# Performance work log

Measured on AMD Instinct MI355X. Metric: run time of the kernel, lower is better.

## Reference

```python
import jax, jax.numpy as jnp
import numpy as np

IFZ = 256      # in_features
SFZ = 1280     # sequence_features
AHZ = 8        # attention heads
AFZ = 64       # attention feature dim per head
NRES = 20      # canonical_num_residues
SCALE = float(np.sqrt(AFZ))
RESID = float(np.sqrt(2.0))
EPS = 1e-6


def _ln(x, s, b, eps=1e-5):
    m = jnp.mean(x, axis=-1, keepdims=True)
    v = jnp.var(x, axis=-1, keepdims=True)
    return (x - m) / jnp.sqrt(v + eps) * s + b


def setup_inputs() -> dict:
    key = jax.random.key(0)
    ks = jax.random.split(key, 20)
    N, B, S = 4096, 4, 512
    HD = AHZ * AFZ
    w = lambda k, shp: (jax.random.normal(k, shp, jnp.float32) * 0.02)
    d = {}
    d["x"] = jax.random.normal(ks[0], (N, IFZ), jnp.float32)
    d["packed_sequence_emb"] = jax.random.normal(ks[1], (B, S, SFZ), jnp.float32)
    d["packed_sequence_mask"] = jnp.ones((B, S), jnp.float32)
    d["prot_mask"] = jnp.arange(N, dtype=jnp.int32)
    d["batch"] = jax.random.randint(ks[2], (N,), 0, B, jnp.int32)
    # projections (bias=False)
    d["Wq"] = w(ks[3], (HD, IFZ))
    d["Wk"] = w(ks[4], (HD, SFZ))
    d["Wv"] = w(ks[5], (HD, SFZ))
    # ag: LayerNorm(HD) -> Linear(HD, IFZ, bias=False) (dropout = identity at eval)
    d["ag_ln_s"] = jnp.ones((HD,), jnp.float32)
    d["ag_ln_b"] = jnp.zeros((HD,), jnp.float32)
    d["Wag"] = w(ks[6], (IFZ, HD))
    d["res_ln_s"] = jnp.ones((3, IFZ), jnp.float32)
    d["res_ln_b"] = jnp.zeros((3, IFZ), jnp.float32)
    d["res_w1"] = w(ks[7], (3, IFZ, IFZ))
    d["res_b1"] = jnp.zeros((3, IFZ), jnp.float32)
    d["res_w2"] = w(ks[8], (3, IFZ, IFZ))
    d["res_b2"] = jnp.zeros((3, IFZ), jnp.float32)
    d["head_w"] = w(ks[9], (NRES, IFZ))
    d["head_b"] = jnp.zeros((NRES,), jnp.float32)
    # output LayerNorm en
    d["en_s"] = jnp.ones((IFZ,), jnp.float32)
    d["en_b"] = jnp.zeros((IFZ,), jnp.float32)
    return d


def _forward(x, emb, mask, prot_mask, batch, Wq, Wk, Wv, ag_ln_s, ag_ln_b, Wag,
             res_ln_s, res_ln_b, res_w1, res_b1, res_w2, res_b2,
             head_w, head_b, en_s, en_b):
    N = x.shape[0]
    B, S = emb.shape[:2]
    b_idx = batch[prot_mask]                      # [M]
    xp = x[prot_mask]                             # [M, IFZ]
    M = xp.shape[0]
    q = (xp @ Wq.T).reshape(M, AHZ, AFZ)          # [M,H,D]
    k = (emb @ Wk.T).reshape(B, S, AHZ, AFZ)      # [B,S,H,D]
    v = (emb @ Wv.T).reshape(B, S, AHZ, AFZ)
    # score vs every protein, then pick own protein (avoids materializing [M,S,H,D] gather)
    scores_all = jnp.einsum('mhd,bshd->mbsh', q, k) / SCALE          # [M,B,S,H]
    sel = b_idx[:, None, None, None]
    scores = jnp.take_along_axis(scores_all, sel, axis=1)[:, 0]       # [M,S,H]
    mb = mask[b_idx][:, :, None]                                      # [M,S,1]
    # padded_sequence_softmax: softmax over S, zero pads, renormalize
    sm = jax.nn.softmax(scores, axis=1) * mb
    w = sm / (jnp.sum(sm, axis=1, keepdims=True) + EPS)               # [M,S,H]
    feat_all = jnp.einsum('msh,bshd->mbhd', w, v)                     # [M,B,H,D]
    feat = jnp.take_along_axis(feat_all, sel, axis=1)[:, 0]
    feat = feat.reshape(M, AHZ * AFZ)
    ag = _ln(feat, ag_ln_s, ag_ln_b) @ Wag.T                          # [M, IFZ]
    # seq_aa_head on the scattered new features (identical to ag for unique prot_mask)
    h = ag
    for i in range(3):
        y = _ln(h, res_ln_s[i], res_ln_b[i])
        y = jax.nn.relu(y @ res_w1[i].T + res_b1[i])
        y = y @ res_w2[i].T + res_b2[i]
        h = (h + y) / RESID
    logits = h @ head_w.T + head_b                                     # [M, NRES]
    new_features = jnp.zeros_like(x).at[prot_mask].set(ag)
    seq_aa_logits = jnp.zeros((N, NRES), x.dtype).at[prot_mask].set(logits)
    unpacked_scores = jnp.zeros((N, S, AHZ), x.dtype).at[prot_mask].set(scores)
    out_x = _ln(x + new_features / RESID, en_s, en_b)
    return out_x, seq_aa_logits, unpacked_scores


def reference(x, packed_sequence_emb, packed_sequence_mask, prot_mask, batch,
              Wq, Wk, Wv, ag_ln_s, ag_ln_b, Wag,
              res_ln_s, res_ln_b, res_w1, res_b1, res_w2, res_b2,
              head_w, head_b, en_s, en_b):
    return _forward(x, packed_sequence_emb, packed_sequence_mask, prot_mask, batch,
                    Wq, Wk, Wv, ag_ln_s, ag_ln_b, Wag,
                    res_ln_s, res_ln_b, res_w1, res_b1, res_w2, res_b2,
                    head_w, head_b, en_s, en_b)
```

## Files before the change

kernel.cpp:

```cpp
#include <hip/hip_runtime.h>
#include <math.h>


typedef short bf8 __attribute__((ext_vector_type(8)));
typedef short bf4 __attribute__((ext_vector_type(4)));
typedef float f32x4 __attribute__((ext_vector_type(4)));
typedef unsigned short u16;

constexpr int LDT = 40;
enum { EPI_NONE = 0, EPI_BIAS_RELU = 1, EPI_BIAS = 2, EPI_RESID = 3 };
#define RSQRT2 0.70710678118654752f

__device__ __forceinline__ u16 f2bf(float f) {
  unsigned int u = __builtin_bit_cast(unsigned int, f);
  unsigned int r = u + 0x7fffu + ((u >> 16) & 1u);
  return (u16)(r >> 16);
}
__device__ __forceinline__ float bf2f(u16 v) {
  return __builtin_bit_cast(float, (unsigned int)v << 16);
}
__device__ __forceinline__ f32x4 mfma16(bf8 a, bf8 b, f32x4 c) {
  return __builtin_amdgcn_mfma_f32_16x16x32_bf16(a, b, c, 0, 0, 0);
}

struct CvtDesc { const float* src; u16* dst; int n; };
struct CvtArgs { CvtDesc d[8]; };

__global__ __launch_bounds__(256) void cvt_k(CvtArgs a) {
  CvtDesc d = a.d[blockIdx.z];
  int i = (blockIdx.x * 256 + threadIdx.x) * 8;
  if (i >= d.n) return;
  f32x4 v0 = *(const f32x4*)(d.src + i);
  f32x4 v1 = *(const f32x4*)(d.src + i + 4);
  bf8 o;
  o[0] = (short)f2bf(v0[0]); o[1] = (short)f2bf(v0[1]);
  o[2] = (short)f2bf(v0[2]); o[3] = (short)f2bf(v0[3]);
  o[4] = (short)f2bf(v1[0]); o[5] = (short)f2bf(v1[1]);
  o[6] = (short)f2bf(v1[2]); o[7] = (short)f2bf(v1[3]);
  *(bf8*)(d.dst + i) = o;
}

template <int EPI, bool BFOUT>
__global__ __launch_bounds__(256) void mgemm2(
    const u16* __restrict__ A, const u16* __restrict__ B,
    void* __restrict__ Cv, int M, int N, int K, int lda, int ldb, int ldc,
    const float* __restrict__ bias, const float* __restrict__ Hin,
    const int* __restrict__ gatherA, const int* __restrict__ scatterC) {
  __shared__ __align__(16) u16 As[128 * LDT];
  __shared__ __align__(16) u16 Bs[64 * LDT];
  const int tid = threadIdx.x;
  const int m0 = blockIdx.y * 128, n0 = blockIdx.x * 64;
  const int wave = tid >> 6, lane = tid & 63;
  const int wm = (wave & 1) * 64, wn = (wave >> 1) * 32;
  const int lrow = lane & 15, quad = lane >> 4;
  const int srow = tid >> 2, skq = tid & 3;

  int gr0 = m0 + srow, gr1 = m0 + srow + 64;
  int ar0 = (gr0 < M) ? (gatherA ? gatherA[gr0] : gr0) : -1;
  int ar1 = (gr1 < M) ? (gatherA ? gatherA[gr1] : gr1) : -1;
  const u16* Ap0 = (ar0 >= 0) ? A + (size_t)ar0 * lda + skq * 8 : nullptr;
  const u16* Ap1 = (ar1 >= 0) ? A + (size_t)ar1 * lda + skq * 8 : nullptr;
  const u16* Bp = (n0 + srow < N) ? B + (size_t)(n0 + srow) * ldb + skq * 8 : nullptr;
  u16* AsW0 = &As[srow * LDT + skq * 8];
  u16* AsW1 = &As[(srow + 64) * LDT + skq * 8];
  u16* BsW = &Bs[srow * LDT + skq * 8];

  f32x4 acc[4][2];
#pragma unroll
  for (int i = 0; i < 4; ++i)
#pragma unroll
    for (int j = 0; j < 2; ++j) acc[i][j] = (f32x4){0.f, 0.f, 0.f, 0.f};
  const bf8 z8 = {0, 0, 0, 0, 0, 0, 0, 0};

  for (int k0 = 0; k0 < K; k0 += 32) {
    bf8 a0 = Ap0 ? *(const bf8*)(Ap0 + k0) : z8;
    bf8 a1 = Ap1 ? *(const bf8*)(Ap1 + k0) : z8;
    bf8 bv = Bp ? *(const bf8*)(Bp + k0) : z8;
    *(bf8*)AsW0 = a0;
    *(bf8*)AsW1 = a1;
    *(bf8*)BsW = bv;
    __syncthreads();
    bf8 af[4], bfr[2];
#pragma unroll
    for (int i = 0; i < 4; ++i)
      af[i] = *(const bf8*)&As[(wm + i * 16 + lrow) * LDT + quad * 8];
#pragma unroll
    for (int j = 0; j < 2; ++j)
      bfr[j] = *(const bf8*)&Bs[(wn + j * 16 + lrow) * LDT + quad * 8];
#pragma unroll
    for (int i = 0; i < 4; ++i)
#pragma unroll
      for (int j = 0; j < 2; ++j) acc[i][j] = mfma16(af[i], bfr[j], acc[i][j]);
    __syncthreads();
  }

  float* Cf = (float*)Cv;
  u16* Cb = (u16*)Cv;
#pragma unroll
  for (int i = 0; i < 4; ++i) {
#pragma unroll
    for (int r = 0; r < 4; ++r) {
      int row = m0 + wm + i * 16 + quad * 4 + r;
      if (row >= M) continue;
      if (gatherA && gatherA[row] < 0) continue;
      int orow = scatterC ? scatterC[row] : row;
#pragma unroll
      for (int j = 0; j < 2; ++j) {
        int col = n0 + wn + j * 16 + lrow;
        if (col >= N) continue;
        float v = acc[i][j][r];
        if (EPI == EPI_BIAS_RELU) v = fmaxf(v + bias[col], 0.f);
        else if (EPI == EPI_BIAS) v += bias[col];
        else if (EPI == EPI_RESID) v = (Hin[(size_t)row * ldc + col] + v + bias[col]) * RSQRT2;
        if (BFOUT) Cb[(size_t)orow * ldc + col] = f2bf(v);
        else Cf[(size_t)orow * ldc + col] = v;
      }
    }
  }
}

__global__ __launch_bounds__(256) void vtrans(const u16* __restrict__ KV,
                                              u16* __restrict__ VT) {
  __shared__ u16 t[32][33];
  int b = blockIdx.z;
  int s0 = blockIdx.x * 32, d0 = blockIdx.y * 32;
  int tx = threadIdx.x & 31, ty = threadIdx.x >> 5;
#pragma unroll
  for (int i = 0; i < 32; i += 8)
    t[ty + i][tx] = KV[(size_t)(b * 512 + s0 + ty + i) * 1024 + 512 + d0 + tx];
  __syncthreads();
#pragma unroll
  for (int i = 0; i < 32; i += 8)
    VT[(size_t)(b * 512 + d0 + ty + i) * 512 + s0 + tx] = t[tx][ty + i];
}

constexpr int WST = 520;
constexpr int QST = 72;

__global__ __launch_bounds__(256) void attn_fused(
    const u16* __restrict__ Q, const u16* __restrict__ KV,
    const u16* __restrict__ VT, const int* __restrict__ list,
    const float* __restrict__ mask, u16* __restrict__ packed,
    u16* __restrict__ feat, int N) {
  const int b = blockIdx.y >> 3, h = blockIdx.y & 7;
  const int mt = blockIdx.x;
  const int* lst = list + (size_t)b * N + mt * 32;
  if (lst[0] < 0) return;

  __shared__ __align__(16) u16 Ws[32 * WST];
  __shared__ __align__(16) u16 Qs[32 * QST];
  __shared__ __align__(16) u16 KVs[64 * QST];
  __shared__ __align__(16) float mk[8][68];
  __shared__ int mS[32];

  const int tid = threadIdx.x;
  const int wave = tid >> 6, lane = tid & 63;
  const int wm = (wave & 1) * 16, wns = (wave >> 1) * 32;
  const int lrow = lane & 15, quad = lane >> 4;
  const bf8 z8 = {0, 0, 0, 0, 0, 0, 0, 0};

  if (tid < 32) mS[tid] = lst[tid];
  {
    int p = tid >> 5, j = (tid & 31) * 2;
    *(float2*)&mk[p][j] = *(const float2*)&mask[(size_t)b * 512 + p * 64 + j];
  }
  {
    int qr = tid >> 3, kq = tid & 7;
    int m = lst[qr];
    *(bf8*)&Qs[qr * QST + kq * 8] =
        (m >= 0) ? *(const bf8*)(Q + (size_t)m * 512 + h * 64 + kq * 8) : z8;
  }
  __syncthreads();

  const bf8 qa0 = *(const bf8*)&Qs[(wm + lrow) * QST + 0 + quad * 8];
  const bf8 qa1 = *(const bf8*)&Qs[(wm + lrow) * QST + 32 + quad * 8];

  const u16* KVb = KV + (size_t)(b * 512) * 1024 + h * 64;
  for (int st = 0; st < 8; ++st) {
#pragma unroll
    for (int i = 0; i < 2; ++i) {
      int c = tid * 2 + i;
      int sr = c >> 3, kq = c & 7;
      *(bf8*)&KVs[sr * QST + kq * 8] =
          *(const bf8*)(KVb + (size_t)(st * 64 + sr) * 1024 + kq * 8);
    }
    __syncthreads();
    f32x4 acc0 = {0.f, 0.f, 0.f, 0.f}, acc1 = acc0;
    {
      bf8 b00 = *(const bf8*)&KVs[(wns + lrow) * QST + quad * 8];
      bf8 b10 = *(const bf8*)&KVs[(wns + 16 + lrow) * QST + quad * 8];
      bf8 b01 = *(const bf8*)&KVs[(wns + lrow) * QST + 32 + quad * 8];
      bf8 b11 = *(const bf8*)&KVs[(wns + 16 + lrow) * QST + 32 + quad * 8];
      acc0 = mfma16(qa0, b00, acc0);
      acc1 = mfma16(qa0, b10, acc1);
      acc0 = mfma16(qa1, b01, acc0);
      acc1 = mfma16(qa1, b11, acc1);
    }
#pragma unroll
    for (int r = 0; r < 4; ++r) {
      int lr = wm + quad * 4 + r;
      Ws[lr * WST + st * 64 + wns + lrow] = f2bf(acc0[r] * 0.125f);
      Ws[lr * WST + st * 64 + wns + 16 + lrow] = f2bf(acc1[r] * 0.125f);
    }
    __syncthreads();
  }

  {
    const int row = tid >> 3, part = tid & 7;
    u16* wrow = &Ws[row * WST + part * 64];
    const int mm = mS[row];
    bf8 w[8];
    float mx = -1e30f;
#pragma unroll
    for (int v = 0; v < 8; ++v) {
      w[v] = *(const bf8*)(wrow + v * 8);
#pragma unroll
      for (int j = 0; j < 8; ++j) mx = fmaxf(mx, bf2f((u16)w[v][j]));
    }
    if (mm >= 0) {
      u16* prow = packed + ((size_t)h * N + mm) * 512 + part * 64;
#pragma unroll
      for (int v = 0; v < 8; ++v) *(bf8*)(prow + v * 8) = w[v];
    }
#pragma unroll
    for (int d = 1; d < 8; d <<= 1) mx = fmaxf(mx, __shfl_xor(mx, d));
    float se = 0.f, ms = 0.f;
#pragma unroll
    for (int v = 0; v < 8; ++v) {
      f32x4 m0 = *(const f32x4*)&mk[part][v * 8];
      f32x4 m1 = *(const f32x4*)&mk[part][v * 8 + 4];
#pragma unroll
      for (int j = 0; j < 8; ++j) {
        float e = __expf(bf2f((u16)w[v][j]) - mx);
        se += e;
        ms += e * (j < 4 ? m0[j] : m1[j - 4]);
      }
    }
#pragma unroll
    for (int d = 1; d < 8; d <<= 1) {
      se += __shfl_xor(se, d);
      ms += __shfl_xor(ms, d);
    }
    float iv = 1.0f / (ms + 1e-6f * se);
#pragma unroll
    for (int v = 0; v < 8; ++v) {
      f32x4 m0 = *(const f32x4*)&mk[part][v * 8];
      f32x4 m1 = *(const f32x4*)&mk[part][v * 8 + 4];
      bf8 o;
#pragma unroll
      for (int j = 0; j < 8; ++j) {
        float e = __expf(bf2f((u16)w[v][j]) - mx);
        o[j] = (short)f2bf(e * (j < 4 ? m0[j] : m1[j - 4]) * iv);
      }
      *(bf8*)(wrow + v * 8) = o;
    }
  }
  __syncthreads();

  f32x4 acc0 = {0.f, 0.f, 0.f, 0.f}, acc1 = acc0;
  const u16* VTb = VT + (size_t)(b * 512 + h * 64) * 512;
  for (int s0 = 0; s0 < 512; s0 += 64) {
#pragma unroll
    for (int i = 0; i < 2; ++i) {
      int c = tid * 2 + i;
      int sr = c >> 3, kq = c & 7;
      *(bf8*)&KVs[sr * QST + kq * 8] =
          *(const bf8*)(VTb + (size_t)sr * 512 + s0 + kq * 8);
    }
    __syncthreads();
#pragma unroll
    for (int k0 = 0; k0 < 64; k0 += 32) {
      bf8 a = *(const bf8*)&Ws[(wm + lrow) * WST + s0 + k0 + quad * 8];
      bf8 b0 = *(const bf8*)&KVs[(wns + lrow) * QST + k0 + quad * 8];
      bf8 b1 = *(const bf8*)&KVs[(wns + 16 + lrow) * QST + k0 + quad * 8];
      acc0 = mfma16(a, b0, acc0);
      acc1 = mfma16(a, b1, acc1);
    }
    __syncthreads();
  }
#pragma unroll
  for (int r = 0; r < 4; ++r) {
    int lr = wm + quad * 4 + r;
    int mm = mS[lr];
    if (mm < 0) continue;
    u16* frow = feat + (size_t)mm * 512 + h * 64;
    frow[wns + lrow] = f2bf(acc0[r]);
    frow[wns + 16 + lrow] = f2bf(acc1[r]);
  }
}

__global__ __launch_bounds__(256) void unpack_k(const u16* __restrict__ packed,
                                                const int* __restrict__ pm,
                                                float* __restrict__ out_sc,
                                                int N) {
  __shared__ u16 Ls[8 * 520];
  int m = blockIdx.x, tid = threadIdx.x;
  int h = tid >> 5, c = (tid & 31) * 16;
  const u16* row = packed + ((size_t)h * N + m) * 512 + c;
  *(bf8*)&Ls[h * 520 + c] = *(const bf8*)row;
  *(bf8*)&Ls[h * 520 + c + 8] = *(const bf8*)(row + 8);
  __syncthreads();
  float* orow = out_sc + (size_t)pm[m] * 4096;
#pragma unroll
  for (int i = 0; i < 16; ++i) {
    int e = tid + i * 256;
    orow[e] = bf2f(Ls[(e & 7) * 520 + (e >> 3)]);
  }
}

template <int W, bool BFIN, bool BFOUT>
__global__ __launch_bounds__(256) void ln_k(const void* __restrict__ in,
                                            void* __restrict__ out,
                                            const float* __restrict__ g,
                                            const float* __restrict__ bb) {
  constexpr int PT = W / 256;
  __shared__ float red[256];
  int row = blockIdx.x, tid = threadIdx.x;
  float v[PT];
  float s = 0.f, sq = 0.f;
#pragma unroll
  for (int p = 0; p < PT; ++p) {
    int c = tid + p * 256;
    v[p] = BFIN ? bf2f(((const u16*)in)[(size_t)row * W + c])
                : ((const float*)in)[(size_t)row * W + c];
    s += v[p];
    sq += v[p] * v[p];
  }
  red[tid] = s;
  __syncthreads();
  for (int off = 128; off; off >>= 1) {
    if (tid < off) red[tid] += red[tid + off];
    __syncthreads();
  }
  float mean = red[0] * (1.0f / W);
  __syncthreads();
  red[tid] = sq;
  __syncthreads();
  for (int off = 128; off; off >>= 1) {
    if (tid < off) red[tid] += red[tid + off];
    __syncthreads();
  }
  float var = red[0] * (1.0f / W) - mean * mean;
  float is = 1.0f / sqrtf(var + 1e-5f);
#pragma unroll
  for (int p = 0; p < PT; ++p) {
    int c = tid + p * 256;
    float o = (v[p] - mean) * is * g[c] + bb[c];
    if (BFOUT) ((u16*)out)[(size_t)row * W + c] = f2bf(o);
    else ((float*)out)[(size_t)row * W + c] = o;
  }
}

constexpr int HST = 268;
constexpr int AST = 280;

__global__ __launch_bounds__(256) void mlp_fused(
    const float* __restrict__ AG, const float* __restrict__ rls,
    const float* __restrict__ rlb, const u16* __restrict__ rw1,
    const float* __restrict__ rb1, const u16* __restrict__ rw2,
    const float* __restrict__ rb2, const float* __restrict__ hw,
    const float* __restrict__ hb, const int* __restrict__ pm,
    float* __restrict__ out_lg) {
  __shared__ __align__(16) float Hs[32 * HST];
  __shared__ __align__(16) u16 As[32 * AST];
  const int tid = threadIdx.x;
  const int m0 = blockIdx.x * 32;
  const int wave = tid >> 6, lane = tid & 63;
  const int lrow = lane & 15, quad = lane >> 4;
  const int wn = wave * 64;
  const int row = tid >> 3, part = tid & 7;

#pragma unroll
  for (int v = 0; v < 8; ++v) {
    int c = v * 32 + part * 4;
    *(f32x4*)&Hs[row * HST + c] = *(const f32x4*)&AG[(size_t)(m0 + row) * 256 + c];
  }

  for (int layer = 0; layer < 3; ++layer) {
    __syncthreads();
    {
      float s = 0.f, sq = 0.f;
      f32x4 hv[8];
#pragma unroll
      for (int v = 0; v < 8; ++v) {
        hv[v] = *(const f32x4*)&Hs[row * HST + v * 32 + part * 4];
#pragma unroll
        for (int e = 0; e < 4; ++e) { s += hv[v][e]; sq += hv[v][e] * hv[v][e]; }
      }
#pragma unroll
      for (int d = 1; d < 8; d <<= 1) { s += __shfl_xor(s, d); sq += __shfl_xor(sq, d); }
      float mean = s * (1.0f / 256.0f);
      float var = sq * (1.0f / 256.0f) - mean * mean;
      float is = 1.0f / sqrtf(var + 1e-5f);
      const float* g = rls + layer * 256;
      const float* bb = rlb + layer * 256;
#pragma unroll
      for (int v = 0; v < 8; ++v) {
        int c = v * 32 + part * 4;
        f32x4 gv = *(const f32x4*)&g[c];
        f32x4 bv = *(const f32x4*)&bb[c];
        bf4 o;
#pragma unroll
        for (int e = 0; e < 4; ++e)
          o[e] = (short)f2bf((hv[v][e] - mean) * is * gv[e] + bv[e]);
        *(bf4*)&As[row * AST + c] = o;
      }
    }
    __syncthreads();

    {
      const u16* W = rw1 + (size_t)layer * 65536;
      f32x4 acc[2][4];
#pragma unroll
      for (int i = 0; i < 2; ++i)
#pragma unroll
        for (int j = 0; j < 4; ++j) acc[i][j] = (f32x4){0.f, 0.f, 0.f, 0.f};
#pragma unroll 4
      for (int k0 = 0; k0 < 256; k0 += 32) {
        bf8 a0 = *(const bf8*)&As[lrow * AST + k0 + quad * 8];
        bf8 a1 = *(const bf8*)&As[(16 + lrow) * AST + k0 + quad * 8];
#pragma unroll
        for (int nt = 0; nt < 4; ++nt) {
          bf8 bfr = *(const bf8*)&W[(size_t)(wn + nt * 16 + lrow) * 256 + k0 + quad * 8];
          acc[0][nt] = mfma16(a0, bfr, acc[0][nt]);
          acc[1][nt] = mfma16(a1, bfr, acc[1][nt]);
        }
      }
      __syncthreads();
      const float* b1 = rb1 + layer * 256;
#pragma unroll
      for (int mt = 0; mt < 2; ++mt)
#pragma unroll
        for (int nt = 0; nt < 4; ++nt) {
          int col = wn + nt * 16 + lrow;
          float bias = b1[col];
#pragma unroll
          for (int r = 0; r < 4; ++r) {
            int rr = mt * 16 + quad * 4 + r;
            As[rr * AST + col] = f2bf(fmaxf(acc[mt][nt][r] + bias, 0.f));
          }
        }
    }
    __syncthreads();

    {
      const u16* W = rw2 + (size_t)layer * 65536;
      f32x4 acc[2][4];
#pragma unroll
      for (int i = 0; i < 2; ++i)
#pragma unroll
        for (int j = 0; j < 4; ++j) acc[i][j] = (f32x4){0.f, 0.f, 0.f, 0.f};
#pragma unroll 4
      for (int k0 = 0; k0 < 256; k0 += 32) {
        bf8 a0 = *(const bf8*)&As[lrow * AST + k0 + quad * 8];
        bf8 a1 = *(const bf8*)&As[(16 + lrow) * AST + k0 + quad * 8];
#pragma unroll
        for (int nt = 0; nt < 4; ++nt) {
          bf8 bfr = *(const bf8*)&W[(size_t)(wn + nt * 16 + lrow) * 256 + k0 + quad * 8];
          acc[0][nt] = mfma16(a0, bfr, acc[0][nt]);
          acc[1][nt] = mfma16(a1, bfr, acc[1][nt]);
        }
      }
      const float* b2 = rb2 + layer * 256;
#pragma unroll
      for (int mt = 0; mt < 2; ++mt)
#pragma unroll
        for (int nt = 0; nt < 4; ++nt) {
          int col = wn + nt * 16 + lrow;
          float bias = b2[col];
#pragma unroll
          for (int r = 0; r < 4; ++r) {
            int rr = mt * 16 + quad * 4 + r;
            Hs[rr * HST + col] = (Hs[rr * HST + col] + acc[mt][nt][r] + bias) * RSQRT2;
          }
        }
    }
  }
  __syncthreads();

  {
    int orow = pm[m0 + row];
    const float* hrow = &Hs[row * HST];
    int c2 = part + 16;
    const float* w0 = hw + (size_t)part * 256;
    const float* w1 = hw + (size_t)(part + 8) * 256;
    const float* w2 = hw + (size_t)(part < 4 ? c2 : 0) * 256;
    float l0 = 0.f, l1 = 0.f, l2 = 0.f;
    for (int k = 0; k < 256; k += 4) {
      f32x4 h4 = *(const f32x4*)&hrow[k];
      f32x4 a4 = *(const f32x4*)&w0[k];
      f32x4 b4 = *(const f32x4*)&w1[k];
      f32x4 c4 = *(const f32x4*)&w2[k];
#pragma unroll
      for (int e = 0; e < 4; ++e) {
        l0 += h4[e] * a4[e];
        l1 += h4[e] * b4[e];
        l2 += h4[e] * c4[e];
      }
    }
    out_lg[(size_t)orow * 20 + part] = l0 + hb[part];
    out_lg[(size_t)orow * 20 + part + 8] = l1 + hb[part + 8];
    if (part < 4) out_lg[(size_t)orow * 20 + c2] = l2 + hb[c2];
  }
}

__global__ __launch_bounds__(256) void outx_k(
    const float* __restrict__ x, const float* __restrict__ ag,
    const int* __restrict__ inv, const float* __restrict__ g,
    const float* __restrict__ bb, float* __restrict__ out) {
  __shared__ float red[256];
  int n = blockIdx.x, tid = threadIdx.x;
  int mi = inv[n];
  float v = x[(size_t)n * 256 + tid];
  if (mi >= 0) v += ag[(size_t)mi * 256 + tid] * RSQRT2;
  red[tid] = v;
  __syncthreads();
  for (int off = 128; off; off >>= 1) {
    if (tid < off) red[tid] += red[tid + off];
    __syncthreads();
  }
  float mean = red[0] * (1.0f / 256.0f);
  __syncthreads();
  red[tid] = v * v;
  __syncthreads();
  for (int off = 128; off; off >>= 1) {
    if (tid < off) red[tid] += red[tid + off];
    __syncthreads();
  }
  float var = red[0] * (1.0f / 256.0f) - mean * mean;
  float is = 1.0f / sqrtf(var + 1e-5f);
  out[(size_t)n * 256 + tid] = (v - mean) * is * g[tid] + bb[tid];
}

__global__ void init_idx_k(int* __restrict__ list, int* __restrict__ inv,
                           int* __restrict__ cnt, int N, int B) {
  int i = blockIdx.x * 256 + threadIdx.x;
  if (i < B * N) list[i] = -1;
  if (i < N) inv[i] = -1;
  if (i < B) cnt[i] = 0;
}

__global__ void compact_k(const int* __restrict__ pm,
                          const int* __restrict__ batch, int* __restrict__ list,
                          int* __restrict__ inv, int* __restrict__ cnt, int N) {
  int m = blockIdx.x * 256 + threadIdx.x;
  if (m >= N) return;
  int p = pm[m];
  int b = batch[p];
  int slot = atomicAdd(&cnt[b], 1);
  list[(size_t)b * N + slot] = m;
  inv[p] = m;
}

extern "C" void kernel_launch(void* const* d_in, const int* in_sizes, int n_in,
                              void* d_out, int out_size, void* d_ws,
                              size_t ws_size, hipStream_t stream) {
  const float* x = (const float*)d_in[0];
  const float* emb = (const float*)d_in[1];
  const float* mask = (const float*)d_in[2];
  const int* pm = (const int*)d_in[3];
  const int* batch = (const int*)d_in[4];
  const float* Wq = (const float*)d_in[5];
  const float* Wk = (const float*)d_in[6];
  const float* Wv = (const float*)d_in[7];
  const float* ag_s = (const float*)d_in[8];
  const float* ag_b = (const float*)d_in[9];
  const float* Wag = (const float*)d_in[10];
  const float* rls = (const float*)d_in[11];
  const float* rlb = (const float*)d_in[12];
  const float* rw1 = (const float*)d_in[13];
  const float* rb1 = (const float*)d_in[14];
  const float* rw2 = (const float*)d_in[15];
  const float* rb2 = (const float*)d_in[16];
  const float* hw = (const float*)d_in[17];
  const float* hb = (const float*)d_in[18];
  const float* ens = (const float*)d_in[19];
  const float* enb = (const float*)d_in[20];

  const int N = in_sizes[0] / 256;
  const int B = in_sizes[2] / 512;

  char* wsb = (char*)d_ws;
  u16* embbf = (u16*)(wsb + 0);
  u16* xbf   = (u16*)(wsb + 5242880);
  u16* Wkvbf = (u16*)(wsb + 7340032);
  u16* Wqbf  = (u16*)(wsb + 9961472);
  u16* packed = (u16*)(wsb + 0);
  u16* KVbf   = (u16*)(wsb + 33554432);
  u16* Qbf    = (u16*)(wsb + 37748736);
  u16* VT     = (u16*)(wsb + 41943040);
  u16* featE  = (u16*)(wsb + 44040192);
  u16* LNF = (u16*)(wsb + 33554432);
  float* AG = (float*)(wsb + 37748736);
  u16* Wagbf = (u16*)(wsb + 48234496);
  u16* rw1bf = (u16*)(wsb + 48496640);
  u16* rw2bf = (u16*)(wsb + 48889856);
  int* list  = (int*)(wsb + 49545216);
  int* inv   = (int*)(wsb + 49610752);
  int* cnt   = (int*)(wsb + 49627136);

  float* out_x = (float*)d_out;
  float* out_lg = out_x + (size_t)N * 256;
  float* out_sc = out_lg + (size_t)N * 20;

  CvtArgs ca;
  ca.d[0] = {emb, embbf, 2 * 512 * 1280 * 2};
  ca.d[1] = {x, xbf, 4096 * 256};
  ca.d[2] = {Wk, Wkvbf, 512 * 1280};
  ca.d[3] = {Wv, Wkvbf + 512 * 1280, 512 * 1280};
  ca.d[4] = {Wq, Wqbf, 512 * 256};
  ca.d[5] = {Wag, Wagbf, 256 * 512};
  ca.d[6] = {rw1, rw1bf, 3 * 256 * 256};
  ca.d[7] = {rw2, rw2bf, 3 * 256 * 256};
  cvt_k<<<dim3(1281, 1, 8), 256, 0, stream>>>(ca);
  init_idx_k<<<(B * N + 255) / 256, 256, 0, stream>>>(list, inv, cnt, N, B);
  compact_k<<<(N + 255) / 256, 256, 0, stream>>>(pm, batch, list, inv, cnt, N);

  mgemm2<EPI_NONE, true><<<dim3(16, 16), 256, 0, stream>>>(
      embbf, Wkvbf, KVbf, B * 512, 1024, 1280, 1280, 1280, 1024,
      nullptr, nullptr, nullptr, nullptr);
  mgemm2<EPI_NONE, true><<<dim3(8, 32), 256, 0, stream>>>(
      xbf, Wqbf, Qbf, N, 512, 256, 256, 256, 512,
      nullptr, nullptr, pm, nullptr);
  vtrans<<<dim3(16, 16, B), 256, 0, stream>>>(KVbf, VT);

  attn_fused<<<dim3(N / 32, B * 8), 256, 0, stream>>>(
      Qbf, KVbf, VT, list, mask, packed, featE, N);
  unpack_k<<<N, 256, 0, stream>>>(packed, pm, out_sc, N);

  ln_k<512, true, true><<<N, 256, 0, stream>>>(featE, LNF, ag_s, ag_b);
  mgemm2<EPI_NONE, false><<<dim3(4, 32), 256, 0, stream>>>(
      LNF, Wagbf, AG, N, 256, 512, 512, 512, 256,
      nullptr, nullptr, nullptr, nullptr);

  mlp_fused<<<dim3(N / 32), 256, 0, stream>>>(
      AG, rls, rlb, rw1bf, rb1, rw2bf, rb2, hw, hb, pm, out_lg);

  outx_k<<<N, 256, 0, stream>>>(x, AG, inv, ens, enb, out_x);
}
```

Measured before the change: 347.1 us.

## Fuse ag LayerNorm and Wag projection into MLP kernel with 16-row tiles

```diff
diff --git a/kernel.cpp b/kernel.cpp
--- a/kernel.cpp
+++ b/kernel.cpp
@@ -3,7 +3,6 @@
 
 
 typedef short bf8 __attribute__((ext_vector_type(8)));
-typedef short bf4 __attribute__((ext_vector_type(4)));
 typedef float f32x4 __attribute__((ext_vector_type(4)));
 typedef unsigned short u16;
 
@@ -308,199 +307,175 @@
   }
 }
 
-template <int W, bool BFIN, bool BFOUT>
-__global__ __launch_bounds__(256) void ln_k(const void* __restrict__ in,
-                                            void* __restrict__ out,
-                                            const float* __restrict__ g,
-                                            const float* __restrict__ bb) {
-  constexpr int PT = W / 256;
-  __shared__ float red[256];
-  int row = blockIdx.x, tid = threadIdx.x;
-  float v[PT];
-  float s = 0.f, sq = 0.f;
-#pragma unroll
-  for (int p = 0; p < PT; ++p) {
-    int c = tid + p * 256;
-    v[p] = BFIN ? bf2f(((const u16*)in)[(size_t)row * W + c])
-                : ((const float*)in)[(size_t)row * W + c];
-    s += v[p];
-    sq += v[p] * v[p];
-  }
-  red[tid] = s;
-  __syncthreads();
-  for (int off = 128; off; off >>= 1) {
-    if (tid < off) red[tid] += red[tid + off];
-    __syncthreads();
-  }
-  float mean = red[0] * (1.0f / W);
-  __syncthreads();
-  red[tid] = sq;
-  __syncthreads();
-  for (int off = 128; off; off >>= 1) {
-    if (tid < off) red[tid] += red[tid + off];
-    __syncthreads();
-  }
-  float var = red[0] * (1.0f / W) - mean * mean;
-  float is = 1.0f / sqrtf(var + 1e-5f);
-#pragma unroll
-  for (int p = 0; p < PT; ++p) {
-    int c = tid + p * 256;
-    float o = (v[p] - mean) * is * g[c] + bb[c];
-    if (BFOUT) ((u16*)out)[(size_t)row * W + c] = f2bf(o);
-    else ((float*)out)[(size_t)row * W + c] = o;
-  }
-}
-
 constexpr int HST = 268;
-constexpr int AST = 280;
-
-__global__ __launch_bounds__(256) void mlp_fused(
-    const float* __restrict__ AG, const float* __restrict__ rls,
+constexpr int AST = 520;
+constexpr int YST = 280;
+
+__global__ __launch_bounds__(512) void mlp_fused(
+    const u16* __restrict__ feat, const float* __restrict__ ag_s,
+    const float* __restrict__ ag_b, const u16* __restrict__ Wag,
+    float* __restrict__ AGout, const float* __restrict__ rls,
     const float* __restrict__ rlb, const u16* __restrict__ rw1,
     const float* __restrict__ rb1, const u16* __restrict__ rw2,
     const float* __restrict__ rb2, const float* __restrict__ hw,
     const float* __restrict__ hb, const int* __restrict__ pm,
     float* __restrict__ out_lg) {
-  __shared__ __align__(16) float Hs[32 * HST];
-  __shared__ __align__(16) u16 As[32 * AST];
+  __shared__ __align__(16) float Hs[16 * HST];
+  __shared__ __align__(16) u16 As[16 * AST];
+  __shared__ __align__(16) u16 Ys[16 * YST];
   const int tid = threadIdx.x;
-  const int m0 = blockIdx.x * 32;
+  const int m0 = blockIdx.x * 16;
   const int wave = tid >> 6, lane = tid & 63;
   const int lrow = lane & 15, quad = lane >> 4;
-  const int wn = wave * 64;
-  const int row = tid >> 3, part = tid & 7;
-
-#pragma unroll
-  for (int v = 0; v < 8; ++v) {
-    int c = v * 32 + part * 4;
-    *(f32x4*)&Hs[row * HST + c] = *(const f32x4*)&AG[(size_t)(m0 + row) * 256 + c];
+  const int wn = wave * 32;
+  const int row = tid >> 5, part = tid & 31;
+
+  {
+    const u16* frow = feat + (size_t)(m0 + row) * 512 + part * 16;
+    bf8 f0 = *(const bf8*)frow;
+    bf8 f1 = *(const bf8*)(frow + 8);
+    float s = 0.f, sq = 0.f;
+#pragma unroll
+    for (int j = 0; j < 8; ++j) {
+      float a = bf2f((u16)f0[j]), b = bf2f((u16)f1[j]);
+      s += a + b;
+      sq += a * a + b * b;
+    }
+#pragma unroll
+    for (int d = 1; d < 32; d <<= 1) { s += __shfl_xor(s, d); sq += __shfl_xor(sq, d); }
+    float mean = s * (1.0f / 512.0f);
+    float var = sq * (1.0f / 512.0f) - mean * mean;
+    float is = 1.0f / sqrtf(var + 1e-5f);
+    int c = part * 16;
+    bf8 o0, o1;
+#pragma unroll
+    for (int j = 0; j < 8; ++j) {
+      o0[j] = (short)f2bf((bf2f((u16)f0[j]) - mean) * is * ag_s[c + j] + ag_b[c + j]);
+      o1[j] = (short)f2bf((bf2f((u16)f1[j]) - mean) * is * ag_s[c + 8 + j] + ag_b[c + 8 + j]);
+    }
+    *(bf8*)&As[row * AST + c] = o0;
+    *(bf8*)&As[row * AST + c + 8] = o1;
+  }
+  __syncthreads();
+
+  {
+    f32x4 acc0 = {0.f, 0.f, 0.f, 0.f}, acc1 = acc0;
+#pragma unroll 4
+    for (int k0 = 0; k0 < 512; k0 += 32) {
+      bf8 a = *(const bf8*)&As[lrow * AST + k0 + quad * 8];
+      bf8 w0 = *(const bf8*)&Wag[(size_t)(wn + lrow) * 512 + k0 + quad * 8];
+      bf8 w1 = *(const bf8*)&Wag[(size_t)(wn + 16 + lrow) * 512 + k0 + quad * 8];
+      acc0 = mfma16(a, w0, acc0);
+      acc1 = mfma16(a, w1, acc1);
+    }
+#pragma unroll
+    for (int r = 0; r < 4; ++r) {
+      int rr = quad * 4 + r;
+      Hs[rr * HST + wn + lrow] = acc0[r];
+      Hs[rr * HST + wn + 16 + lrow] = acc1[r];
+      AGout[(size_t)(m0 + rr) * 256 + wn + lrow] = acc0[r];
+      AGout[(size_t)(m0 + rr) * 256 + wn + 16 + lrow] = acc1[r];
+    }
   }
 
   for (int layer = 0; layer < 3; ++layer) {
     __syncthreads();
     {
+      int c = part * 8;
+      f32x4 h0 = *(const f32x4*)&Hs[row * HST + c];
+      f32x4 h1 = *(const f32x4*)&Hs[row * HST + c + 4];
       float s = 0.f, sq = 0.f;
-      f32x4 hv[8];
-#pragma unroll
-      for (int v = 0; v < 8; ++v) {
-        hv[v] = *(const f32x4*)&Hs[row * HST + v * 32 + part * 4];
-#pragma unroll
-        for (int e = 0; e < 4; ++e) { s += hv[v][e]; sq += hv[v][e] * hv[v][e]; }
-      }
-#pragma unroll
-      for (int d = 1; d < 8; d <<= 1) { s += __shfl_xor(s, d); sq += __shfl_xor(sq, d); }
+#pragma unroll
+      for (int e = 0; e < 4; ++e) {
+        s += h0[e] + h1[e];
+        sq += h0[e] * h0[e] + h1[e] * h1[e];
+      }
+#pragma unroll
+      for (int d = 1; d < 32; d <<= 1) { s += __shfl_xor(s, d); sq += __shfl_xor(sq, d); }
       float mean = s * (1.0f / 256.0f);
       float var = sq * (1.0f / 256.0f) - mean * mean;
       float is = 1.0f / sqrtf(var + 1e-5f);
       const float* g = rls + layer * 256;
       const float* bb = rlb + layer * 256;
-#pragma unroll
-      for (int v = 0; v < 8; ++v) {
-        int c = v * 32 + part * 4;
-        f32x4 gv = *(const f32x4*)&g[c];
-        f32x4 bv = *(const f32x4*)&bb[c];
-        bf4 o;
-#pragma unroll
-        for (int e = 0; e < 4; ++e)
-          o[e] = (short)f2bf((hv[v][e] - mean) * is * gv[e] + bv[e]);
-        *(bf4*)&As[row * AST + c] = o;
-      }
+      bf8 o;
+#pragma unroll
+      for (int e = 0; e < 4; ++e) {
+        o[e] = (short)f2bf((h0[e] - mean) * is * g[c + e] + bb[c + e]);
+        o[e + 4] = (short)f2bf((h1[e] - mean) * is * g[c + 4 + e] + bb[c + 4 + e]);
+      }
+      *(bf8*)&As[row * AST + c] = o;
     }
     __syncthreads();
 
     {
       const u16* W = rw1 + (size_t)layer * 65536;
-      f32x4 acc[2][4];
-#pragma unroll
-      for (int i = 0; i < 2; ++i)
-#pragma unroll
-        for (int j = 0; j < 4; ++j) acc[i][j] = (f32x4){0.f, 0.f, 0.f, 0.f};
+      f32x4 acc0 = {0.f, 0.f, 0.f, 0.f}, acc1 = acc0;
 #pragma unroll 4
       for (int k0 = 0; k0 < 256; k0 += 32) {
-        bf8 a0 = *(const bf8*)&As[lrow * AST + k0 + quad * 8];
-        bf8 a1 = *(const bf8*)&As[(16 + lrow) * AST + k0 + quad * 8];
-#pragma unroll
-        for (int nt = 0; nt < 4; ++nt) {
-          bf8 bfr = *(const bf8*)&W[(size_t)(wn + nt * 16 + lrow) * 256 + k0 + quad * 8];
-          acc[0][nt] = mfma16(a0, bfr, acc[0][nt]);
-          acc[1][nt] = mfma16(a1, bfr, acc[1][nt]);
-        }
-      }
-      __syncthreads();
+        bf8 a = *(const bf8*)&As[lrow * AST + k0 + quad * 8];
+        bf8 w0 = *(const bf8*)&W[(size_t)(wn + lrow) * 256 + k0 + quad * 8];
+        bf8 w1 = *(const bf8*)&W[(size_t)(wn + 16 + lrow) * 256 + k0 + quad * 8];
+        acc0 = mfma16(a, w0, acc0);
+        acc1 = mfma16(a, w1, acc1);
+      }
       const float* b1 = rb1 + layer * 256;
-#pragma unroll
-      for (int mt = 0; mt < 2; ++mt)
-#pragma unroll
-        for (int nt = 0; nt < 4; ++nt) {
-          int col = wn + nt * 16 + lrow;
-          float bias = b1[col];
-#pragma unroll
-          for (int r = 0; r < 4; ++r) {
-            int rr = mt * 16 + quad * 4 + r;
-            As[rr * AST + col] = f2bf(fmaxf(acc[mt][nt][r] + bias, 0.f));
-          }
-        }
+      float bi0 = b1[wn + lrow], bi1 = b1[wn + 16 + lrow];
+#pragma unroll
+      for (int r = 0; r < 4; ++r) {
+        int rr = quad * 4 + r;
+        Ys[rr * YST + wn + lrow] = f2bf(fmaxf(acc0[r] + bi0, 0.f));
+        Ys[rr * YST + wn + 16 + lrow] = f2bf(fmaxf(acc1[r] + bi1, 0.f));
+      }
     }
     __syncthreads();
 
     {
       const u16* W = rw2 + (size_t)layer * 65536;
-      f32x4 acc[2][4];
-#pragma unroll
-      for (int i = 0; i < 2; ++i)
-#pragma unroll
-        for (int j = 0; j < 4; ++j) acc[i][j] = (f32x4){0.f, 0.f, 0.f, 0.f};
+      f32x4 acc0 = {0.f, 0.f, 0.f, 0.f}, acc1 = acc0;
 #pragma unroll 4
       for (int k0 = 0; k0 < 256; k0 += 32) {
-        bf8 a0 = *(const bf8*)&As[lrow * AST + k0 + quad * 8];
-        bf8 a1 = *(const bf8*)&As[(16 + lrow) * AST + k0 + quad * 8];
-#pragma unroll
-        for (int nt = 0; nt < 4; ++nt) {
-          bf8 bfr = *(const bf8*)&W[(size_t)(wn + nt * 16 + lrow) * 256 + k0 + quad * 8];
-          acc[0][nt] = mfma16(a0, bfr, acc[0][nt]);
-          acc[1][nt] = mfma16(a1, bfr, acc[1][nt]);
-        }
+        bf8 a = *(const bf8*)&Ys[lrow * YST + k0 + quad * 8];
+        bf8 w0 = *(const bf8*)&W[(size_t)(wn + lrow) * 256 + k0 + quad * 8];
+        bf8 w1 = *(const bf8*)&W[(size_t)(wn + 16 + lrow) * 256 + k0 + quad * 8];
+        acc0 = mfma16(a, w0, acc0);
+        acc1 = mfma16(a, w1, acc1);
       }
       const float* b2 = rb2 + layer * 256;
-#pragma unroll
-      for (int mt = 0; mt < 2; ++mt)
-#pragma unroll
-        for (int nt = 0; nt < 4; ++nt) {
-          int col = wn + nt * 16 + lrow;
-          float bias = b2[col];
-#pragma unroll
-          for (int r = 0; r < 4; ++r) {
-            int rr = mt * 16 + quad * 4 + r;
-            Hs[rr * HST + col] = (Hs[rr * HST + col] + acc[mt][nt][r] + bias) * RSQRT2;
-          }
-        }
-    }
-  }
-  __syncthreads();
-
-  {
-    int orow = pm[m0 + row];
+      float bi0 = b2[wn + lrow], bi1 = b2[wn + 16 + lrow];
+#pragma unroll
+      for (int r = 0; r < 4; ++r) {
+        int rr = quad * 4 + r;
+        float* h0 = &Hs[rr * HST + wn + lrow];
+        float* h1 = &Hs[rr * HST + wn + 16 + lrow];
+        *h0 = (*h0 + acc0[r] + bi0) * RSQRT2;
+        *h1 = (*h1 + acc1[r] + bi1) * RSQRT2;
+      }
+    }
+  }
+  __syncthreads();
+
+  if (part < 20) {
     const float* hrow = &Hs[row * HST];
-    int c2 = part + 16;
-    const float* w0 = hw + (size_t)part * 256;
-    const float* w1 = hw + (size_t)(part + 8) * 256;
-    const float* w2 = hw + (size_t)(part < 4 ? c2 : 0) * 256;
-    float l0 = 0.f, l1 = 0.f, l2 = 0.f;
-    for (int k = 0; k < 256; k += 4) {
-      f32x4 h4 = *(const f32x4*)&hrow[k];
-      f32x4 a4 = *(const f32x4*)&w0[k];
-      f32x4 b4 = *(const f32x4*)&w1[k];
-      f32x4 c4 = *(const f32x4*)&w2[k];
+    const float* wrow = hw + (size_t)part * 256;
+    float l0 = 0.f, l1 = 0.f, l2 = 0.f, l3 = 0.f;
+    for (int k = 0; k < 256; k += 16) {
+      f32x4 h0 = *(const f32x4*)&hrow[k];
+      f32x4 h1 = *(const f32x4*)&hrow[k + 4];
+      f32x4 h2 = *(const f32x4*)&hrow[k + 8];
+      f32x4 h3 = *(const f32x4*)&hrow[k + 12];
+      f32x4 w0 = *(const f32x4*)&wrow[k];
+      f32x4 w1 = *(const f32x4*)&wrow[k + 4];
+      f32x4 w2 = *(const f32x4*)&wrow[k + 8];
+      f32x4 w3 = *(const f32x4*)&wrow[k + 12];
 #pragma unroll
       for (int e = 0; e < 4; ++e) {
-        l0 += h4[e] * a4[e];
-        l1 += h4[e] * b4[e];
-        l2 += h4[e] * c4[e];
-      }
-    }
-    out_lg[(size_t)orow * 20 + part] = l0 + hb[part];
-    out_lg[(size_t)orow * 20 + part + 8] = l1 + hb[part + 8];
-    if (part < 4) out_lg[(size_t)orow * 20 + c2] = l2 + hb[c2];
+        l0 += h0[e] * w0[e];
+        l1 += h1[e] * w1[e];
+        l2 += h2[e] * w2[e];
+        l3 += h3[e] * w3[e];
+      }
+    }
+    out_lg[(size_t)pm[m0 + row] * 20 + part] = l0 + l1 + l2 + l3 + hb[part];
   }
 }
 
@@ -590,7 +565,6 @@
   u16* Qbf    = (u16*)(wsb + 37748736);
   u16* VT     = (u16*)(wsb + 41943040);
   u16* featE  = (u16*)(wsb + 44040192);
-  u16* LNF = (u16*)(wsb + 33554432);
   float* AG = (float*)(wsb + 37748736);
   u16* Wagbf = (u16*)(wsb + 48234496);
   u16* rw1bf = (u16*)(wsb + 48496640);
@@ -628,13 +602,9 @@
       Qbf, KVbf, VT, list, mask, packed, featE, N);
   unpack_k<<<N, 256, 0, stream>>>(packed, pm, out_sc, N);
 
-  ln_k<512, true, true><<<N, 256, 0, stream>>>(featE, LNF, ag_s, ag_b);
-  mgemm2<EPI_NONE, false><<<dim3(4, 32), 256, 0, stream>>>(
-      LNF, Wagbf, AG, N, 256, 512, 512, 512, 256,
-      nullptr, nullptr, nullptr, nullptr);
-
-  mlp_fused<<<dim3(N / 32), 256, 0, stream>>>(
-      AG, rls, rlb, rw1bf, rb1, rw2bf, rb2, hw, hb, pm, out_lg);
+  mlp_fused<<<dim3(N / 16), 512, 0, stream>>>(
+      featE, ag_s, ag_b, Wagbf, AG, rls, rlb, rw1bf, rb1, rw2bf, rb2,
+      hw, hb, pm, out_lg);
 
   outx_k<<<N, 256, 0, stream>>>(x, AG, inv, ens, enb, out_x);
 }
```

New measurement: 310.5 us. 1.12x faster.
